# Kernel tuning notes

Hardware: AMD Instinct MI355X
Metric: run time of the kernel (lower is better)

Reference implementation:

```python
import jax, jax.numpy as jnp
import numpy as np

T, IN_DIM, HID, OUT = 4096, 768, 768, 4

def setup_inputs() -> dict:
    key = jax.random.key(0)
    ks = jax.random.split(key, 5)
    s_i = 1.0 / np.sqrt(IN_DIM)
    s_h = 1.0 / np.sqrt(HID)
    return {
        "inputs": jax.random.normal(ks[0], (T, IN_DIM), jnp.float32),
        "h0": jnp.zeros((HID,), jnp.float32),
        "Wi": jax.random.normal(ks[1], (IN_DIM, 3 * HID), jnp.float32) * s_i,
        "bi": jnp.zeros((3 * HID,), jnp.float32),
        "Wh": jax.random.normal(ks[2], (HID, 3 * HID), jnp.float32) * s_h,
        "bhn": jnp.zeros((HID,), jnp.float32),
        "Wd": jax.random.normal(ks[3], (HID, OUT), jnp.float32) * s_h,
        "bd": jnp.zeros((OUT,), jnp.float32),
    }

def reference(inputs, h0, Wi, bi, Wh, bhn, Wd, bd):
    H = h0.shape[-1]
    # Precompute all input projections in one big GEMM: [T, 3H]
    xi_all = inputs @ Wi + bi

    def step(h, xi):
        hh = h @ Wh  # [3H]
        xr, xz, xn = xi[:H], xi[H:2 * H], xi[2 * H:]
        hr, hz, hn = hh[:H], hh[H:2 * H], hh[2 * H:]
        r = jax.nn.sigmoid(xr + hr)
        z = jax.nn.sigmoid(xz + hz)
        n = jnp.tanh(xn + r * (hn + bhn))
        h_new = (1.0 - z) * n + z * h  # flax GRUCell update
        return h_new, h_new

    final_h, y = jax.lax.scan(step, h0, xi_all)  # y: [T, H]
    output = y @ Wd + bd  # [T, OUT]
    rng = jax.random.key(42)
    rng, act_rng = jax.random.split(rng)
    action = jax.random.categorical(act_rng, output[:, :2])  # [T]
    return output, action, final_h
```

## Files before the change

kernel.cpp:

```cpp
#include <hip/hip_runtime.h>
#include <stdint.h>

#define T_STEPS 4096
#define HID     768
#define G3      2304
#define NBLK    192
#define NTHR    192
#define UPB     4

__device__ __forceinline__ void threefry2x32(uint32_t k0, uint32_t k1,
                                             uint32_t x0, uint32_t x1,
                                             uint32_t* o0, uint32_t* o1) {
  uint32_t ks0 = k0, ks1 = k1, ks2 = k0 ^ k1 ^ 0x1BD11BDAu;
  uint32_t ks[3] = {ks0, ks1, ks2};
  x0 += ks[0]; x1 += ks[1];
  const int r0[4] = {13, 15, 26, 6};
  const int r1[4] = {17, 29, 16, 24};
#pragma unroll
  for (int i = 0; i < 5; ++i) {
    const int* rr = (i & 1) ? r1 : r0;
#pragma unroll
    for (int j = 0; j < 4; ++j) {
      x0 += x1;
      x1 = (x1 << rr[j]) | (x1 >> (32 - rr[j]));
      x1 ^= x0;
    }
    x0 += ks[(i + 1) % 3];
    x1 += ks[(i + 2) % 3] + (uint32_t)(i + 1);
  }
  *o0 = x0; *o1 = x1;
}

__device__ __forceinline__ float gumbel_from_bits(uint32_t bits) {
  float f = __uint_as_float((bits >> 9) | 0x3f800000u) - 1.0f;
  float u = fmaxf(f, 1.17549435e-38f);
  return -logf(-logf(u));
}

__global__ void init_pairs(const float* __restrict__ h0,
                           unsigned long long* __restrict__ pairs) {
  int j = threadIdx.x;
  if (j < HID) {
    pairs[j]        = (unsigned long long)__float_as_uint(h0[j]);
    pairs[HID + j]  = 0xFFFFFFFF00000000ull;
  }
}

__launch_bounds__(256)
__global__ void gemm_xi(const float* __restrict__ A, const float* __restrict__ B,
                        const float* __restrict__ bias, float* __restrict__ C) {
  const int N = G3, K = HID;
  __shared__ __align__(16) float As[8][128];
  __shared__ __align__(16) float Bs[8][128];
  int tid = threadIdx.x;
  int bn = blockIdx.x * 128;
  int bm = blockIdx.y * 128;
  int tx = tid & 15, ty = tid >> 4;

  float acc[8][8];
#pragma unroll
  for (int i = 0; i < 8; ++i)
#pragma unroll
    for (int j = 0; j < 8; ++j) acc[i][j] = 0.f;

  const int ar = tid >> 1;
  const int ac = (tid & 1) * 4;
  const int br = tid >> 5;
  const int bc = (tid & 31) * 4;
  const float* Aptr = A + (size_t)(bm + ar) * K + ac;
  const float* Bptr = B + (size_t)br * N + bn + bc;

  for (int k0 = 0; k0 < K; k0 += 8) {
    float4 av = *(const float4*)(Aptr + k0);
    float4 bv = *(const float4*)(Bptr + (size_t)k0 * N);
    As[ac + 0][ar] = av.x; As[ac + 1][ar] = av.y;
    As[ac + 2][ar] = av.z; As[ac + 3][ar] = av.w;
    *(float4*)&Bs[br][bc] = bv;
    __syncthreads();
#pragma unroll
    for (int kk = 0; kk < 8; ++kk) {
      float a[8], b[8];
      *(float4*)&a[0] = *(const float4*)&As[kk][ty * 8];
      *(float4*)&a[4] = *(const float4*)&As[kk][ty * 8 + 4];
      *(float4*)&b[0] = *(const float4*)&Bs[kk][tx * 8];
      *(float4*)&b[4] = *(const float4*)&Bs[kk][tx * 8 + 4];
#pragma unroll
      for (int i = 0; i < 8; ++i)
#pragma unroll
        for (int j = 0; j < 8; ++j) acc[i][j] = fmaf(a[i], b[j], acc[i][j]);
    }
    __syncthreads();
  }
#pragma unroll
  for (int i = 0; i < 8; ++i) {
    float* crow = C + (size_t)(bm + ty * 8 + i) * N + bn + tx * 8;
    const float* brow = bias + bn + tx * 8;
#pragma unroll
    for (int j = 0; j < 8; ++j) crow[j] = acc[i][j] + brow[j];
  }
}

__launch_bounds__(NTHR)
__global__ void gru_scan(const float* __restrict__ xi, const float* __restrict__ Wh,
                         const float* __restrict__ bhn,
                         unsigned long long* __restrict__ pairs,
                         float* __restrict__ y) {
  __shared__ __align__(16) float h_lds[16 * 52];
  __shared__ float dots[12];

  const int tid = threadIdx.x;
  const int b = blockIdx.x;
  const int g = tid >> 4;
  const int l = tid & 15;
  const int u0 = b * UPB;

  const int C = (g < 4) ? (u0 + g)
              : (g < 8) ? (HID + u0 + (g - 4))
                        : (2 * HID + u0 + (g - 8));

  float w[48];
#pragma unroll
  for (int i = 0; i < 48; ++i) w[i] = Wh[(size_t)(l * 48 + i) * G3 + C];

  float bhn_u = 0.f;
  if (tid < UPB) bhn_u = bhn[u0 + tid];

  const int base_k = tid * 4;

  for (int t = 0; t < T_STEPS; ++t) {
    unsigned long long* buf = pairs + (size_t)(t & 1) * HID;

    float xr = 0.f, xz = 0.f, xn = 0.f;
    if (tid < UPB) {
      const float* xrow = xi + (size_t)t * G3;
      xr = xrow[u0 + tid];
      xz = xrow[HID + u0 + tid];
      xn = xrow[2 * HID + u0 + tid];
    }

    unsigned int got = 0;
    while (got != 0xFu) {
#pragma unroll
      for (int c = 0; c < 4; ++c) {
        if (!(got & (1u << c))) {
          unsigned long long v = __hip_atomic_load(&buf[base_k + c], __ATOMIC_RELAXED,
                                                   __HIP_MEMORY_SCOPE_AGENT);
          if ((int)(v >> 32) == t) {
            int k = base_k + c;
            h_lds[k + 4 * (k / 48)] = __uint_as_float((unsigned int)v);
            got |= (1u << c);
          }
        }
      }
      if (got != 0xFu) __builtin_amdgcn_s_sleep(1);
    }
    __syncthreads();

    float a0 = 0.f, a1 = 0.f, a2 = 0.f, a3 = 0.f;
    const float4* hp = (const float4*)&h_lds[52 * l];
#pragma unroll
    for (int i = 0; i < 12; ++i) {
      float4 h4 = hp[i];
      a0 = fmaf(w[4 * i + 0], h4.x, a0);
      a1 = fmaf(w[4 * i + 1], h4.y, a1);
      a2 = fmaf(w[4 * i + 2], h4.z, a2);
      a3 = fmaf(w[4 * i + 3], h4.w, a3);
    }
    float acc = (a0 + a1) + (a2 + a3);
    acc += __shfl_xor(acc, 8, 16);
    acc += __shfl_xor(acc, 4, 16);
    acc += __shfl_xor(acc, 2, 16);
    acc += __shfl_xor(acc, 1, 16);
    if (l == 0) dots[g] = acc;

    float hprev = 0.f;
    if (tid < UPB) {
      int j = u0 + tid;
      hprev = h_lds[j + 4 * (j / 48)];
    }
    __syncthreads();

    if (tid < UPB) {
      float hr = dots[tid], hz = dots[4 + tid], hn = dots[8 + tid];
      float r = 1.f / (1.f + expf(-(xr + hr)));
      float z = 1.f / (1.f + expf(-(xz + hz)));
      float n = tanhf(xn + r * (hn + bhn_u));
      float hnew = (1.f - z) * n + z * hprev;
      int j = u0 + tid;
      y[(size_t)t * HID + j] = hnew;
      unsigned long long pv =
          (((unsigned long long)(unsigned int)(t + 1)) << 32) | __float_as_uint(hnew);
      __hip_atomic_store(&pairs[(size_t)((t + 1) & 1) * HID + j], pv, __ATOMIC_RELAXED,
                         __HIP_MEMORY_SCOPE_AGENT);
    }
    __syncthreads();
  }
}

__launch_bounds__(256)
__global__ void decode_out(const float* __restrict__ y, const float* __restrict__ Wd,
                           const float* __restrict__ bd, float* __restrict__ out) {
  int tid = threadIdx.x;
  int lane = tid & 63;
  int wid = tid >> 6;
  int r = blockIdx.x * 4 + wid;
  const float* yr = y + (size_t)r * HID;

  float acc0 = 0.f, acc1 = 0.f, acc2 = 0.f, acc3 = 0.f;
#pragma unroll
  for (int i = 0; i < 12; ++i) {
    int k = lane + 64 * i;
    float yv = yr[k];
    float4 wd = *(const float4*)&Wd[(size_t)k * 4];
    acc0 = fmaf(yv, wd.x, acc0);
    acc1 = fmaf(yv, wd.y, acc1);
    acc2 = fmaf(yv, wd.z, acc2);
    acc3 = fmaf(yv, wd.w, acc3);
    if (r == T_STEPS - 1) out[20480 + k] = yv;
  }
#pragma unroll
  for (int m = 32; m >= 1; m >>= 1) {
    acc0 += __shfl_xor(acc0, m, 64);
    acc1 += __shfl_xor(acc1, m, 64);
    acc2 += __shfl_xor(acc2, m, 64);
    acc3 += __shfl_xor(acc3, m, 64);
  }
  if (lane == 0) {
    float o0 = acc0 + bd[0], o1 = acc1 + bd[1], o2 = acc2 + bd[2], o3 = acc3 + bd[3];
    out[(size_t)r * 4 + 0] = o0;
    out[(size_t)r * 4 + 1] = o1;
    out[(size_t)r * 4 + 2] = o2;
    out[(size_t)r * 4 + 3] = o3;

    uint32_t ak0, ak1;
    threefry2x32(0u, 42u, 0u, 1u, &ak0, &ak1);
    uint32_t s0, s1;
    threefry2x32(ak0, ak1, 0u, (uint32_t)(2 * r), &s0, &s1);
    uint32_t g0bits = s0 ^ s1;
    threefry2x32(ak0, ak1, 0u, (uint32_t)(2 * r + 1), &s0, &s1);
    uint32_t g1bits = s0 ^ s1;

    float gg0 = gumbel_from_bits(g0bits);
    float gg1 = gumbel_from_bits(g1bits);
    int action = (o1 + gg1 > o0 + gg0) ? 1 : 0;
    out[16384 + r] = (float)action;
  }
}

extern "C" void kernel_launch(void* const* d_in, const int* in_sizes, int n_in,
                              void* d_out, int out_size, void* d_ws, size_t ws_size,
                              hipStream_t stream) {
  const float* inputs = (const float*)d_in[0];
  const float* h0     = (const float*)d_in[1];
  const float* Wi     = (const float*)d_in[2];
  const float* bi     = (const float*)d_in[3];
  const float* Wh     = (const float*)d_in[4];
  const float* bhn    = (const float*)d_in[5];
  const float* Wd     = (const float*)d_in[6];
  const float* bd     = (const float*)d_in[7];
  float* out = (float*)d_out;

  char* ws = (char*)d_ws;
  unsigned long long* pairs = (unsigned long long*)ws;
  float* xi = (float*)(ws + 16384);
  float* y  = (float*)(ws + 16384 + (size_t)T_STEPS * G3 * 4);

  hipLaunchKernelGGL(init_pairs, dim3(1), dim3(HID), 0, stream, h0, pairs);
  hipLaunchKernelGGL(gemm_xi, dim3(G3 / 128, T_STEPS / 128), dim3(256), 0, stream,
                     inputs, Wi, bi, xi);

  {
    const float* xi_c = xi;
    const float* wh_c = Wh;
    const float* bhn_c = bhn;
    unsigned long long* pr = pairs;
    float* y_p = y;
    void* args[] = { (void*)&xi_c, (void*)&wh_c, (void*)&bhn_c, (void*)&pr, (void*)&y_p };
    hipError_t e = hipLaunchCooperativeKernel((const void*)gru_scan, dim3(NBLK),
                                              dim3(NTHR), args, 0, stream);
    if (e != hipSuccess) {
      hipLaunchKernelGGL(gru_scan, dim3(NBLK), dim3(NTHR), 0, stream,
                         xi_c, wh_c, bhn_c, pr, y_p);
    }
  }

  hipLaunchKernelGGL(decode_out, dim3(T_STEPS / 4), dim3(256), 0, stream, y, Wd, bd, out);
}
```

Measured before the change: 10.56 ms.

## Poll recurrent state with vectorized sc1 loads, fast activations, publish before y store

```diff
diff --git a/kernel.cpp b/kernel.cpp
--- a/kernel.cpp
+++ b/kernel.cpp
@@ -7,12 +7,14 @@
 #define NBLK    192
 #define NTHR    192
 #define UPB     4
+#define FAST_SWEEPS 512
+
+typedef unsigned int uintv4 __attribute__((ext_vector_type(4)));
 
 __device__ __forceinline__ void threefry2x32(uint32_t k0, uint32_t k1,
                                              uint32_t x0, uint32_t x1,
                                              uint32_t* o0, uint32_t* o1) {
-  uint32_t ks0 = k0, ks1 = k1, ks2 = k0 ^ k1 ^ 0x1BD11BDAu;
-  uint32_t ks[3] = {ks0, ks1, ks2};
+  uint32_t ks[3] = {k0, k1, k0 ^ k1 ^ 0x1BD11BDAu};
   x0 += ks[0]; x1 += ks[1];
   const int r0[4] = {13, 15, 26, 6};
   const int r1[4] = {17, 29, 16, 24};
@@ -37,12 +39,20 @@
   return -logf(-logf(u));
 }
 
+__device__ __forceinline__ float fast_sigmoid(float x) {
+  return 1.0f / (1.0f + __expf(-x));
+}
+__device__ __forceinline__ float fast_tanh(float x) {
+  float e = __expf(2.0f * x);
+  return 1.0f - 2.0f / (e + 1.0f);
+}
+
 __global__ void init_pairs(const float* __restrict__ h0,
                            unsigned long long* __restrict__ pairs) {
   int j = threadIdx.x;
   if (j < HID) {
-    pairs[j]        = (unsigned long long)__float_as_uint(h0[j]);
-    pairs[HID + j]  = 0xFFFFFFFF00000000ull;
+    pairs[j]       = (unsigned long long)__float_as_uint(h0[j]);
+    pairs[HID + j] = 0xFFFFFFFF00000000ull;
   }
 }
 
@@ -126,6 +136,7 @@
   if (tid < UPB) bhn_u = bhn[u0 + tid];
 
   const int base_k = tid * 4;
+  bool use_fb = false;
 
   for (int t = 0; t < T_STEPS; ++t) {
     unsigned long long* buf = pairs + (size_t)(t & 1) * HID;
@@ -138,21 +149,52 @@
       xn = xrow[2 * HID + u0 + tid];
     }
 
-    unsigned int got = 0;
-    while (got != 0xFu) {
-#pragma unroll
-      for (int c = 0; c < 4; ++c) {
-        if (!(got & (1u << c))) {
-          unsigned long long v = __hip_atomic_load(&buf[base_k + c], __ATOMIC_RELAXED,
-                                                   __HIP_MEMORY_SCOPE_AGENT);
-          if ((int)(v >> 32) == t) {
-            int k = base_k + c;
-            h_lds[k + 4 * (k / 48)] = __uint_as_float((unsigned int)v);
-            got |= (1u << c);
+    {
+      const unsigned long long* p = &buf[base_k];
+      bool done = false;
+      if (!use_fb) {
+        int it = 0;
+        do {
+          uintv4 q;
+          asm volatile("global_load_dwordx4 %0, %1, off sc1\n\t"
+                       "s_waitcnt vmcnt(0)"
+                       : "=&v"(q) : "v"(p) : "memory");
+          if (q[1] == (unsigned int)t && q[3] == (unsigned int)t) {
+            uintv4 q2;
+            asm volatile("global_load_dwordx4 %0, %1, off sc1\n\t"
+                         "s_waitcnt vmcnt(0)"
+                         : "=&v"(q2) : "v"(p + 2) : "memory");
+            if (q2[1] == (unsigned int)t && q2[3] == (unsigned int)t) {
+              int k = base_k;
+              h_lds[k + 0 + 4 * ((k + 0) / 48)] = __uint_as_float(q[0]);
+              h_lds[k + 1 + 4 * ((k + 1) / 48)] = __uint_as_float(q[2]);
+              h_lds[k + 2 + 4 * ((k + 2) / 48)] = __uint_as_float(q2[0]);
+              h_lds[k + 3 + 4 * ((k + 3) / 48)] = __uint_as_float(q2[2]);
+              done = true;
+              break;
+            }
+          }
+        } while (++it < FAST_SWEEPS);
+        if (!done) use_fb = true;
+      }
+      if (!done) {
+        unsigned int got = 0;
+        while (got != 0xFu) {
+#pragma unroll
+          for (int c = 0; c < 4; ++c) {
+            if (!(got & (1u << c))) {
+              unsigned long long v = __hip_atomic_load(&buf[base_k + c],
+                                                       __ATOMIC_RELAXED,
+                                                       __HIP_MEMORY_SCOPE_AGENT);
+              if ((int)(v >> 32) == t) {
+                int k = base_k + c;
+                h_lds[k + 4 * (k / 48)] = __uint_as_float((unsigned int)v);
+                got |= (1u << c);
+              }
+            }
           }
         }
       }
-      if (got != 0xFu) __builtin_amdgcn_s_sleep(1);
     }
     __syncthreads();
 
@@ -182,16 +224,16 @@
 
     if (tid < UPB) {
       float hr = dots[tid], hz = dots[4 + tid], hn = dots[8 + tid];
-      float r = 1.f / (1.f + expf(-(xr + hr)));
-      float z = 1.f / (1.f + expf(-(xz + hz)));
-      float n = tanhf(xn + r * (hn + bhn_u));
+      float r = fast_sigmoid(xr + hr);
+      float z = fast_sigmoid(xz + hz);
+      float n = fast_tanh(xn + r * (hn + bhn_u));
       float hnew = (1.f - z) * n + z * hprev;
       int j = u0 + tid;
-      y[(size_t)t * HID + j] = hnew;
       unsigned long long pv =
           (((unsigned long long)(unsigned int)(t + 1)) << 32) | __float_as_uint(hnew);
       __hip_atomic_store(&pairs[(size_t)((t + 1) & 1) * HID + j], pv, __ATOMIC_RELAXED,
                          __HIP_MEMORY_SCOPE_AGENT);
+      y[(size_t)t * HID + j] = hnew;
     }
     __syncthreads();
   }
```

After: 9.182 ms (median of 2 runs). 13.1% less time.
